# Performance work log

Measured on AMD Instinct MI355X. Metric: run time of the kernel, lower is better.

Reference implementation:

```python
import jax, jax.numpy as jnp
import numpy as np

HUMAN_IDX = 0
SCORE_TH = 0.2
NMS_TH = 0.5
MIN_H, MAX_H = 3, 15
MIN_O, MAX_O = 3, 15
NEG = -1e9


def cxcywh_to_xyxy(b):
    cx, cy, w, h = jnp.split(b, 4, axis=-1)
    return jnp.concatenate([cx - 0.5 * w, cy - 0.5 * h, cx + 0.5 * w, cy + 0.5 * h], -1)


def pairwise_iou(a, b):
    # torchvision-style IoU treating last-dim-4 as xyxy (areas unclamped, mimics
    # batched_nms being fed cxcywh boxes exactly as the original module does).
    lt = jnp.maximum(a[:, None, :2], b[None, :, :2])
    rb = jnp.minimum(a[:, None, 2:], b[None, :, 2:])
    wh = jnp.clip(rb - lt, 0.0)
    inter = wh[..., 0] * wh[..., 1]
    area_a = (a[:, 2] - a[:, 0]) * (a[:, 3] - a[:, 1])
    area_b = (b[:, 2] - b[:, 0]) * (b[:, 3] - b[:, 1])
    union = area_a[:, None] + area_b[None, :] - inter
    return inter / jnp.where(union == 0, 1.0, union)


def nms_keep(boxes, scores, labels, iou_th):
    # batched_nms via the class-offset trick, greedy suppression in score order
    Q = boxes.shape[0]
    off = labels.astype(boxes.dtype)[:, None] * (boxes.max() + 1.0)
    b = boxes + off
    order = jnp.argsort(-scores)
    bs = b[order]
    iou = pairwise_iou(bs, bs)                      # [Q,Q]
    later = jnp.arange(Q)[None, :] > jnp.arange(Q)[:, None]
    sup_mat = (iou > iou_th) & later

    def body(i, keep):
        return keep & ~(sup_mat[i] & keep[i])

    keep_sorted = jax.lax.fori_loop(0, Q, body, jnp.ones(Q, dtype=bool))
    return jnp.zeros(Q, dtype=bool).at[order].set(keep_sorted)


def decode_boxes(b, d):
    # BoxPairCoder-style delta decode on normalized cxcywh boxes
    cx, cy, w, h = b[:, 0], b[:, 1], b[:, 2], b[:, 3]
    cx2 = cx + d[:, 0] * w
    cy2 = cy + d[:, 1] * h
    w2 = w * jnp.exp(d[:, 2])
    h2 = h * jnp.exp(d[:, 3])
    return jnp.stack([cx2, cy2, w2, h2], -1)


def per_image(logits, boxes, hs, size, Wv, bv, Wb, bb):
    prob = jax.nn.softmax(logits, -1)
    scores = prob[:, :-1].max(-1)
    labels = jnp.argmax(prob[:, :-1], -1)
    keep = nms_keep(boxes, scores, labels, NMS_TH)

    is_h = labels == HUMAN_IDX
    h_sc = jnp.where(keep & is_h, scores, NEG)
    o_sc = jnp.where(keep & ~is_h, scores, NEG)
    n_h = jnp.sum(keep & is_h & (scores >= SCORE_TH))
    n_o = jnp.sum(keep & ~is_h & (scores >= SCORE_TH))
    k_h = jnp.clip(n_h, MIN_H, MAX_H)
    k_o = jnp.clip(n_o, MIN_O, MAX_O)

    top_h_sc, idx_h = jax.lax.top_k(h_sc, MAX_H)
    top_o_sc, idx_o = jax.lax.top_k(o_sc, MAX_O)
    val_h = (jnp.arange(MAX_H) < k_h) & (top_h_sc > NEG / 2)
    val_o = (jnp.arange(MAX_O) < k_o) & (top_o_sc > NEG / 2)

    # all human-object pairs [P = MAX_H*MAX_O]
    ih = jnp.repeat(idx_h, MAX_O)
    io = jnp.tile(idx_o, MAX_H)
    pair_valid = jnp.repeat(val_h, MAX_O) & jnp.tile(val_o, MAX_H)

    feat = jnp.concatenate([hs[ih], hs[io]], -1)    # [P, 2D]
    vlog = feat @ Wv + bv                           # verb logits [P, V]
    delta = feat @ Wb + bb                          # box-pair deltas [P, 8]

    pr = (jnp.repeat(jnp.where(val_h, top_h_sc, 0.0), MAX_O)
          * jnp.tile(jnp.where(val_o, top_o_sc, 0.0), MAX_H))
    pr = jnp.where(pair_valid, pr, 0.0)

    bh = decode_boxes(boxes[ih], delta[:, :4])
    bo = decode_boxes(boxes[io], delta[:, 4:])

    hgt, wid = size[0], size[1]
    scale = jnp.stack([wid, hgt, wid, hgt])
    kept = jnp.concatenate([idx_h, idx_o])
    boxes_out = cxcywh_to_xyxy(boxes[kept]) * scale
    bh_out = cxcywh_to_xyxy(bh) * scale
    bo_out = cxcywh_to_xyxy(bo) * scale
    det_scores = jax.nn.sigmoid(vlog) * pr[:, None]
    return boxes_out, bh_out, bo_out, det_scores


def setup_inputs() -> dict:
    key = jax.random.key(0)
    ks = jax.random.split(key, 6)
    B, Q, C1, D, V = 64, 900, 81, 256, 117
    return {
        "pred_logits": jax.random.normal(ks[0], (B, Q, C1), jnp.float32),
        "pred_boxes": jax.random.uniform(ks[1], (B, Q, 4), jnp.float32),
        "hidden_states": jax.random.normal(ks[2], (B, Q, D), jnp.float32),
        "image_sizes": jax.random.uniform(ks[3], (B, 2), jnp.float32) * 1000.0 + 300.0,
        "W_verb": jax.random.normal(ks[4], (2 * D, V), jnp.float32) * 0.02,
        "b_verb": jnp.zeros((V,), jnp.float32),
        "W_bbox": jax.random.normal(ks[5], (2 * D, 8), jnp.float32) * 0.02,
        "b_bbox": jnp.zeros((8,), jnp.float32),
    }


def reference(pred_logits, pred_boxes, hidden_states, image_sizes, W_verb, b_verb, W_bbox, b_bbox):
    f = jax.vmap(per_image, in_axes=(0, 0, 0, 0, None, None, None, None))
    return f(pred_logits, pred_boxes, hidden_states, image_sizes, W_verb, b_verb, W_bbox, b_bbox)
```

## Files before the change

kernel.cpp:

```cpp
#include <hip/hip_runtime.h>
#include <math.h>

#define NB 64
#define Q 900
#define NC 81
#define NC2 80
#define HD 256
#define NV 117
#define NEGV -1000000000.0f

static const size_t OFF_SCORES = 0;
static const size_t OFF_LABELS = 230400;
static const size_t OFF_HSC    = 460800;
static const size_t OFF_OSC    = 691200;

typedef float float4u __attribute__((ext_vector_type(4), aligned(4)));

__global__ __launch_bounds__(256) void k_score(const float* __restrict__ logits,
                                               float* __restrict__ scores,
                                               int* __restrict__ labels) {
  int quad = threadIdx.x >> 2, qq = threadIdx.x & 3;
  int row = blockIdx.x * 64 + quad;
  const float* lp = logits + (size_t)row * NC;
  float4u x[5];
  #pragma unroll
  for (int j = 0; j < 5; j++) {
    int c = qq + 4 * j;
    x[j] = *(const float4u*)(lp + c * 4);
  }
  float x80 = (qq == 0) ? lp[80] : -INFINITY;
  float m = x80;
  #pragma unroll
  for (int j = 0; j < 5; j++)
    m = fmaxf(m, fmaxf(fmaxf(x[j].x, x[j].y), fmaxf(x[j].z, x[j].w)));
  m = fmaxf(m, __shfl_xor(m, 1));
  m = fmaxf(m, __shfl_xor(m, 2));
  float e = (qq == 0) ? expf(x80 - m) : 0.0f;
  #pragma unroll
  for (int j = 0; j < 5; j++)
    e += expf(x[j].x - m) + expf(x[j].y - m) + expf(x[j].z - m) + expf(x[j].w - m);
  e += __shfl_xor(e, 1);
  e += __shfl_xor(e, 2);
  float bv = -INFINITY; int bi = 0x7fffffff;
  #pragma unroll
  for (int j = 0; j < 5; j++) {
    int base = (qq + 4 * j) * 4;
    if (x[j].x > bv) { bv = x[j].x; bi = base; }
    if (x[j].y > bv) { bv = x[j].y; bi = base + 1; }
    if (x[j].z > bv) { bv = x[j].z; bi = base + 2; }
    if (x[j].w > bv) { bv = x[j].w; bi = base + 3; }
  }
  #pragma unroll
  for (int s = 1; s <= 2; s <<= 1) {
    float ov = __shfl_xor(bv, s); int oi = __shfl_xor(bi, s);
    if (ov > bv || (ov == bv && oi < bi)) { bv = ov; bi = oi; }
  }
  if (qq == 0) {
    scores[row] = expf(bv - m) / e;
    labels[row] = bi;
  }
}

__global__ __launch_bounds__(512) void k_cnms(const float* __restrict__ scores,
                                              const int* __restrict__ labels,
                                              const float* __restrict__ boxes,
                                              float* __restrict__ hsc,
                                              float* __restrict__ osc) {
#pragma clang fp contract(off)
  int img = blockIdx.x;
  int tid = threadIdx.x;
  int wid = tid >> 6, lane = tid & 63;
  int c = blockIdx.y * 8 + wid;
  size_t imgQ = (size_t)img * Q;
  __shared__ float  s_sc[8][64];
  __shared__ int    s_idx[8][64];
  __shared__ int    s_srt[8][64];
  __shared__ float  s_ssc[8][64];
  __shared__ float4 s_sb[8][64];
  __shared__ unsigned long long s_sup[8][64];
  __shared__ float  s_wmax[8];

  const float4* bp4 = (const float4*)(boxes + imgQ * 4);
  float bm = -INFINITY;
  for (int i = tid; i < Q; i += 512) {
    float4 v = bp4[i];
    bm = fmaxf(bm, fmaxf(fmaxf(v.x, v.y), fmaxf(v.z, v.w)));
  }
  #pragma unroll
  for (int s = 32; s > 0; s >>= 1) bm = fmaxf(bm, __shfl_xor(bm, s));
  if (lane == 0) s_wmax[wid] = bm;
  __syncthreads();
  float bmax = s_wmax[0];
  #pragma unroll
  for (int i = 1; i < 8; i++) bmax = fmaxf(bmax, s_wmax[i]);

  int lb[15]; float sc[15];
  #pragma unroll
  for (int e = 0; e < 15; e++) {
    int i = e * 64 + lane;
    lb[e] = (i < Q) ? labels[imgQ + i] : -1;
    sc[e] = (i < Q) ? scores[imgQ + i] : 0.0f;
  }
  unsigned long long lmask = (1ull << lane) - 1ull;
  int n = 0;
  #pragma unroll
  for (int e = 0; e < 15; e++) {
    bool memb = (lb[e] == c);
    unsigned long long mm = __ballot(memb);
    if (memb) {
      int pos = n + __popcll(mm & lmask);
      if (pos < 64) { s_idx[wid][pos] = e * 64 + lane; s_sc[wid][pos] = sc[e]; }
    }
    n += __popcll(mm);
  }
  n = min(n, 64);

  int   myidx = (lane < n) ? s_idx[wid][lane] : 0;
  float mysc  = (lane < n) ? s_sc[wid][lane]  : -INFINITY;

  int rank = 0;
  #pragma unroll 4
  for (int j = 0; j < n; j++) {
    float sj = s_sc[wid][j];
    rank += (sj > mysc) || (sj == mysc && j < lane);
  }

  if (lane < n) {
    float off = (float)c * (bmax + 1.0f);
    const float* bp = boxes + (imgQ + myidx) * 4;
    float4 b;
    b.x = bp[0] + off; b.y = bp[1] + off;
    b.z = bp[2] + off; b.w = bp[3] + off;
    s_srt[wid][rank] = myidx;
    s_ssc[wid][rank] = mysc;
    s_sb[wid][rank]  = b;
  }

  float4 mb = (lane < n) ? s_sb[wid][lane] : float4{0.f, 0.f, 0.f, 0.f};
  float areaA = (mb.z - mb.x) * (mb.w - mb.y);

  unsigned long long sup = 0;
  #pragma unroll 4
  for (int j = 0; j < n; j++) {
    float4 cb = s_sb[wid][j];
    if (j > lane && lane < n) {
      float ltx = fmaxf(mb.x, cb.x), lty = fmaxf(mb.y, cb.y);
      float rbx = fminf(mb.z, cb.z), rby = fminf(mb.w, cb.w);
      float ww = fmaxf(rbx - ltx, 0.0f), hh = fmaxf(rby - lty, 0.0f);
      float inter = ww * hh;
      float areaB = (cb.z - cb.x) * (cb.w - cb.y);
      float uni = areaA + areaB - inter;
      float denom = (uni == 0.0f) ? 1.0f : uni;
      if (inter / denom > 0.5f) sup |= (1ull << j);
    }
  }
  s_sup[wid][lane] = sup;

  unsigned long long keepm = (n >= 64) ? ~0ull : ((1ull << n) - 1ull);
  #pragma unroll 4
  for (int i = 0; i < n; i++) {
    unsigned long long row = s_sup[wid][i];
    if ((keepm >> i) & 1ull) keepm &= ~row;
  }

  if (lane < n) {
    int kept = (int)((keepm >> lane) & 1ull);
    int   oi = s_srt[wid][lane];
    float os = s_ssc[wid][lane];
    hsc[imgQ + oi] = (kept && c == 0) ? os : NEGV;
    osc[imgQ + oi] = (kept && c != 0) ? os : NEGV;
  }
}

__global__ __launch_bounds__(512) void k_back(const float* __restrict__ hscg,
                                              const float* __restrict__ oscg,
                                              const float* __restrict__ boxes,
                                              const float* __restrict__ hs,
                                              const float* __restrict__ sizes,
                                              const float* __restrict__ Wv,
                                              const float* __restrict__ bverb,
                                              const float* __restrict__ Wb,
                                              const float* __restrict__ bbox,
                                              float* __restrict__ out) {
  int slice = blockIdx.x, img = blockIdx.y;
  int t = threadIdx.x, w = t >> 6, lane = t & 63;
  size_t imgQ = (size_t)img * Q;

  __shared__ __attribute__((aligned(16))) float s_A[30 * 260];
  __shared__ float s_B[2][64][16];
  __shared__ float s_Cg[30][16];
  __shared__ int   s_tki[30];
  __shared__ float s_tkv[30];
  __shared__ int   s_tkval[30];
  __shared__ float s_pr[225];
  __shared__ float s_box30[120];

  if (w < 2) {
    const float* src = (w == 0) ? hscg : oscg;
    float v[15];
    int cnt = 0;
    #pragma unroll
    for (int e = 0; e < 15; e++) {
      int i = e * 64 + lane;
      float val = (i < Q) ? src[imgQ + i] : -INFINITY;
      cnt += (val >= 0.2f) ? 1 : 0;
      v[e] = val;
    }
    #pragma unroll
    for (int s = 32; s > 0; s >>= 1) cnt += __shfl_xor(cnt, s);

    float selv = 0.f; int seli = 0;
    for (int r = 0; r < 15; r++) {
      float bv_ = -INFINITY; int bi_ = 0x7fffffff;
      #pragma unroll
      for (int e = 0; e < 15; e++) { if (v[e] > bv_) { bv_ = v[e]; bi_ = e * 64 + lane; } }
      #pragma unroll
      for (int s = 32; s > 0; s >>= 1) {
        float ov = __shfl_xor(bv_, s); int oi2 = __shfl_xor(bi_, s);
        if (ov > bv_ || (ov == bv_ && oi2 < bi_)) { bv_ = ov; bi_ = oi2; }
      }
      if (lane == r) { selv = bv_; seli = bi_; }
      if ((bi_ & 63) == lane) {
        int ee = bi_ >> 6;
        #pragma unroll
        for (int e = 0; e < 15; e++) if (e == ee) v[e] = -2.0e9f;
      }
    }
    int kk = min(max(cnt, 3), 15);
    if (lane < 15) {
      s_tki[w * 15 + lane]   = seli;
      s_tkv[w * 15 + lane]   = selv;
      s_tkval[w * 15 + lane] = (lane < kk && selv > -5.0e8f) ? 1 : 0;
    }
  }
  __syncthreads();

  if (t < 225) {
    int h_ = t / 15, o_ = t - h_ * 15;
    float th = s_tkv[h_], to_ = s_tkv[15 + o_];
    s_pr[t] = (s_tkval[h_] && s_tkval[15 + o_]) ? th * to_ : 0.0f;
  }
  if (t < 120) {
    int r = t >> 2, j = t & 3;
    s_box30[t] = boxes[(imgQ + s_tki[r]) * 4 + j];
  }

  for (int f = t; f < 1920; f += 512) {
    int r = f >> 6, q = f & 63;
    float4 a = *(const float4*)(hs + (imgQ + s_tki[r]) * HD + q * 4);
    ((float4*)s_A)[r * 65 + q] = a;
  }

  int r = t >> 4, c = t & 15;
  float acc = 0.0f;
  for (int kc = 0; kc < 256; kc += 64) {
    __syncthreads();
    for (int idx = t; idx < 2048; idx += 512) {
      int half = idx >> 10, rem = idx & 1023;
      int k_l = rem >> 4, c_l = rem & 15;
      int pcol = slice * 16 + c_l;
      int kg = kc + k_l + (half ? 256 : 0);
      float val = 0.0f;
      if (pcol < 117)      val = Wv[(size_t)kg * 117 + pcol];
      else if (pcol < 125) val = Wb[(size_t)kg * 8 + (pcol - 117)];
      s_B[half][k_l][c_l] = val;
    }
    __syncthreads();
    if (r < 30) {
      const float* Bp = &s_B[r < 15 ? 0 : 1][0][0];
      #pragma unroll
      for (int kk = 0; kk < 64; kk += 4) {
        float4 a4 = *(const float4*)(s_A + r * 260 + kc + kk);
        acc += a4.x * Bp[(kk + 0) * 16 + c];
        acc += a4.y * Bp[(kk + 1) * 16 + c];
        acc += a4.z * Bp[(kk + 2) * 16 + c];
        acc += a4.w * Bp[(kk + 3) * 16 + c];
      }
    }
  }
  if (r < 30) s_Cg[r][c] = acc;
  __syncthreads();

  float hgt = sizes[img * 2 + 0], wid = sizes[img * 2 + 1];
  float* out0 = out;
  float* out1 = out + 7680;
  float* out2 = out + 65280;
  float* out3 = out + 122880;

  int veff = (slice < 7) ? 16 : 5;
  for (int e = t; e < 225 * veff; e += 512) {
    int p = e / veff, cl = e - p * veff;
    int ph = p / 15, po = p - ph * 15;
    int v = slice * 16 + cl;
    float x = s_Cg[ph][cl] + s_Cg[15 + po][cl] + bverb[v];
    out3[(size_t)img * 26325 + p * NV + v] = (1.0f / (1.0f + expf(-x))) * s_pr[p];
  }

  if (slice == 7) {
    if (t < 30) {
      const float* bp = s_box30 + t * 4;
      float cx = bp[0], cy = bp[1], ww = bp[2], hh = bp[3];
      float* o = out0 + ((size_t)img * 30 + t) * 4;
      o[0] = (cx - 0.5f * ww) * wid;
      o[1] = (cy - 0.5f * hh) * hgt;
      o[2] = (cx + 0.5f * ww) * wid;
      o[3] = (cy + 0.5f * hh) * hgt;
    }
    if (t < 225) {
      int h_ = t / 15, o_ = t - h_ * 15;
      {
        float d0 = s_Cg[h_][5] + s_Cg[15 + o_][5] + bbox[0];
        float d1 = s_Cg[h_][6] + s_Cg[15 + o_][6] + bbox[1];
        float d2 = s_Cg[h_][7] + s_Cg[15 + o_][7] + bbox[2];
        float d3 = s_Cg[h_][8] + s_Cg[15 + o_][8] + bbox[3];
        const float* bp = s_box30 + h_ * 4;
        float cx = bp[0], cy = bp[1], ww = bp[2], hh = bp[3];
        float cx2 = cx + d0 * ww, cy2 = cy + d1 * hh;
        float w2 = ww * expf(d2), h2 = hh * expf(d3);
        float* o = out1 + ((size_t)img * 225 + t) * 4;
        o[0] = (cx2 - 0.5f * w2) * wid;
        o[1] = (cy2 - 0.5f * h2) * hgt;
        o[2] = (cx2 + 0.5f * w2) * wid;
        o[3] = (cy2 + 0.5f * h2) * hgt;
      }
      {
        float d4 = s_Cg[h_][9]  + s_Cg[15 + o_][9]  + bbox[4];
        float d5 = s_Cg[h_][10] + s_Cg[15 + o_][10] + bbox[5];
        float d6 = s_Cg[h_][11] + s_Cg[15 + o_][11] + bbox[6];
        float d7 = s_Cg[h_][12] + s_Cg[15 + o_][12] + bbox[7];
        const float* bp = s_box30 + (15 + o_) * 4;
        float cx = bp[0], cy = bp[1], ww = bp[2], hh = bp[3];
        float cx2 = cx + d4 * ww, cy2 = cy + d5 * hh;
        float w2 = ww * expf(d6), h2 = hh * expf(d7);
        float* o = out2 + ((size_t)img * 225 + t) * 4;
        o[0] = (cx2 - 0.5f * w2) * wid;
        o[1] = (cy2 - 0.5f * h2) * hgt;
        o[2] = (cx2 + 0.5f * w2) * wid;
        o[3] = (cy2 + 0.5f * h2) * hgt;
      }
    }
  }
}

extern "C" void kernel_launch(void* const* d_in, const int* in_sizes, int n_in,
                              void* d_out, int out_size, void* d_ws, size_t ws_size,
                              hipStream_t stream) {
  const float* logits = (const float*)d_in[0];
  const float* boxes  = (const float*)d_in[1];
  const float* hs     = (const float*)d_in[2];
  const float* sizes  = (const float*)d_in[3];
  const float* Wv     = (const float*)d_in[4];
  const float* bv     = (const float*)d_in[5];
  const float* Wb     = (const float*)d_in[6];
  const float* bb     = (const float*)d_in[7];
  float* out = (float*)d_out;
  char* ws = (char*)d_ws;

  float* scores = (float*)(ws + OFF_SCORES);
  int*   labels = (int*)(ws + OFF_LABELS);
  float* hsc    = (float*)(ws + OFF_HSC);
  float* osc    = (float*)(ws + OFF_OSC);

  k_score<<<900, 256, 0, stream>>>(logits, scores, labels);
  k_cnms<<<dim3(NB, 10), 512, 0, stream>>>(scores, labels, boxes, hsc, osc);
  k_back<<<dim3(8, NB), 512, 0, stream>>>(hsc, osc, boxes, hs, sizes,
                                          Wv, bv, Wb, bb, out);
}
```

Baseline: 54.20 us.

## Fuse score, class-NMS and backend into one persistent kernel with grid barriers

Merges the three kernels into a single 512-block persistent kernel that runs scoring, per-class NMS and the pair head as phases separated by software grid barriers built on atomics, with a memset to reset the barrier counters. The per-image box max moves to a global buffer, and the GEMM is reworked for 256-thread blocks, each thread accumulating two rows. The aim is to remove the inter-kernel launch gaps and tail effects. In exchange it adds barrier spin cost and depends on all 512 blocks being co-resident (launch bounds request 3 blocks per CU); if they are not, the barrier only exits through its guard counter.

```diff
diff --git a/kernel.cpp b/kernel.cpp
--- a/kernel.cpp
+++ b/kernel.cpp
@@ -8,335 +8,378 @@
 #define HD 256
 #define NV 117
 #define NEGV -1000000000.0f
+#define GRID 512
+#define BLK 256
 
 static const size_t OFF_SCORES = 0;
 static const size_t OFF_LABELS = 230400;
 static const size_t OFF_HSC    = 460800;
 static const size_t OFF_OSC    = 691200;
+static const size_t OFF_BMAX   = 921600;
+static const size_t OFF_BAR    = 922112;
 
 typedef float float4u __attribute__((ext_vector_type(4), aligned(4)));
 
-__global__ __launch_bounds__(256) void k_score(const float* __restrict__ logits,
-                                               float* __restrict__ scores,
-                                               int* __restrict__ labels) {
-  int quad = threadIdx.x >> 2, qq = threadIdx.x & 3;
-  int row = blockIdx.x * 64 + quad;
-  const float* lp = logits + (size_t)row * NC;
-  float4u x[5];
-  #pragma unroll
-  for (int j = 0; j < 5; j++) {
-    int c = qq + 4 * j;
-    x[j] = *(const float4u*)(lp + c * 4);
+__device__ __forceinline__ void gridbar(int* cnt, int* flag) {
+  __syncthreads();
+  if (threadIdx.x == 0) {
+    __threadfence();
+    int prev = atomicAdd(cnt, 1);
+    if (prev == GRID - 1) {
+      __hip_atomic_store(flag, 1, __ATOMIC_RELEASE, __HIP_MEMORY_SCOPE_AGENT);
+    } else {
+      int guard = 0;
+      while (__hip_atomic_load(flag, __ATOMIC_ACQUIRE, __HIP_MEMORY_SCOPE_AGENT) == 0
+             && guard < (1 << 24)) {
+        guard++;
+        __builtin_amdgcn_s_sleep(2);
+      }
+    }
+    __threadfence();
   }
-  float x80 = (qq == 0) ? lp[80] : -INFINITY;
-  float m = x80;
-  #pragma unroll
-  for (int j = 0; j < 5; j++)
-    m = fmaxf(m, fmaxf(fmaxf(x[j].x, x[j].y), fmaxf(x[j].z, x[j].w)));
-  m = fmaxf(m, __shfl_xor(m, 1));
-  m = fmaxf(m, __shfl_xor(m, 2));
-  float e = (qq == 0) ? expf(x80 - m) : 0.0f;
-  #pragma unroll
-  for (int j = 0; j < 5; j++)
-    e += expf(x[j].x - m) + expf(x[j].y - m) + expf(x[j].z - m) + expf(x[j].w - m);
-  e += __shfl_xor(e, 1);
-  e += __shfl_xor(e, 2);
-  float bv = -INFINITY; int bi = 0x7fffffff;
-  #pragma unroll
-  for (int j = 0; j < 5; j++) {
-    int base = (qq + 4 * j) * 4;
-    if (x[j].x > bv) { bv = x[j].x; bi = base; }
-    if (x[j].y > bv) { bv = x[j].y; bi = base + 1; }
-    if (x[j].z > bv) { bv = x[j].z; bi = base + 2; }
-    if (x[j].w > bv) { bv = x[j].w; bi = base + 3; }
-  }
-  #pragma unroll
-  for (int s = 1; s <= 2; s <<= 1) {
-    float ov = __shfl_xor(bv, s); int oi = __shfl_xor(bi, s);
-    if (ov > bv || (ov == bv && oi < bi)) { bv = ov; bi = oi; }
-  }
-  if (qq == 0) {
-    scores[row] = expf(bv - m) / e;
-    labels[row] = bi;
-  }
+  __syncthreads();
 }
 
-__global__ __launch_bounds__(512) void k_cnms(const float* __restrict__ scores,
-                                              const int* __restrict__ labels,
-                                              const float* __restrict__ boxes,
-                                              float* __restrict__ hsc,
-                                              float* __restrict__ osc) {
-#pragma clang fp contract(off)
-  int img = blockIdx.x;
-  int tid = threadIdx.x;
-  int wid = tid >> 6, lane = tid & 63;
-  int c = blockIdx.y * 8 + wid;
-  size_t imgQ = (size_t)img * Q;
-  __shared__ float  s_sc[8][64];
-  __shared__ int    s_idx[8][64];
-  __shared__ int    s_srt[8][64];
-  __shared__ float  s_ssc[8][64];
-  __shared__ float4 s_sb[8][64];
-  __shared__ unsigned long long s_sup[8][64];
-  __shared__ float  s_wmax[8];
-
-  const float4* bp4 = (const float4*)(boxes + imgQ * 4);
-  float bm = -INFINITY;
-  for (int i = tid; i < Q; i += 512) {
-    float4 v = bp4[i];
-    bm = fmaxf(bm, fmaxf(fmaxf(v.x, v.y), fmaxf(v.z, v.w)));
-  }
-  #pragma unroll
-  for (int s = 32; s > 0; s >>= 1) bm = fmaxf(bm, __shfl_xor(bm, s));
-  if (lane == 0) s_wmax[wid] = bm;
-  __syncthreads();
-  float bmax = s_wmax[0];
-  #pragma unroll
-  for (int i = 1; i < 8; i++) bmax = fmaxf(bmax, s_wmax[i]);
-
-  int lb[15]; float sc[15];
-  #pragma unroll
-  for (int e = 0; e < 15; e++) {
-    int i = e * 64 + lane;
-    lb[e] = (i < Q) ? labels[imgQ + i] : -1;
-    sc[e] = (i < Q) ? scores[imgQ + i] : 0.0f;
-  }
-  unsigned long long lmask = (1ull << lane) - 1ull;
-  int n = 0;
-  #pragma unroll
-  for (int e = 0; e < 15; e++) {
-    bool memb = (lb[e] == c);
-    unsigned long long mm = __ballot(memb);
-    if (memb) {
-      int pos = n + __popcll(mm & lmask);
-      if (pos < 64) { s_idx[wid][pos] = e * 64 + lane; s_sc[wid][pos] = sc[e]; }
-    }
-    n += __popcll(mm);
-  }
-  n = min(n, 64);
-
-  int   myidx = (lane < n) ? s_idx[wid][lane] : 0;
-  float mysc  = (lane < n) ? s_sc[wid][lane]  : -INFINITY;
-
-  int rank = 0;
-  #pragma unroll 4
-  for (int j = 0; j < n; j++) {
-    float sj = s_sc[wid][j];
-    rank += (sj > mysc) || (sj == mysc && j < lane);
-  }
-
-  if (lane < n) {
-    float off = (float)c * (bmax + 1.0f);
-    const float* bp = boxes + (imgQ + myidx) * 4;
-    float4 b;
-    b.x = bp[0] + off; b.y = bp[1] + off;
-    b.z = bp[2] + off; b.w = bp[3] + off;
-    s_srt[wid][rank] = myidx;
-    s_ssc[wid][rank] = mysc;
-    s_sb[wid][rank]  = b;
-  }
-
-  float4 mb = (lane < n) ? s_sb[wid][lane] : float4{0.f, 0.f, 0.f, 0.f};
-  float areaA = (mb.z - mb.x) * (mb.w - mb.y);
-
-  unsigned long long sup = 0;
-  #pragma unroll 4
-  for (int j = 0; j < n; j++) {
-    float4 cb = s_sb[wid][j];
-    if (j > lane && lane < n) {
-      float ltx = fmaxf(mb.x, cb.x), lty = fmaxf(mb.y, cb.y);
-      float rbx = fminf(mb.z, cb.z), rby = fminf(mb.w, cb.w);
-      float ww = fmaxf(rbx - ltx, 0.0f), hh = fmaxf(rby - lty, 0.0f);
-      float inter = ww * hh;
-      float areaB = (cb.z - cb.x) * (cb.w - cb.y);
-      float uni = areaA + areaB - inter;
-      float denom = (uni == 0.0f) ? 1.0f : uni;
-      if (inter / denom > 0.5f) sup |= (1ull << j);
-    }
-  }
-  s_sup[wid][lane] = sup;
-
-  unsigned long long keepm = (n >= 64) ? ~0ull : ((1ull << n) - 1ull);
-  #pragma unroll 4
-  for (int i = 0; i < n; i++) {
-    unsigned long long row = s_sup[wid][i];
-    if ((keepm >> i) & 1ull) keepm &= ~row;
-  }
-
-  if (lane < n) {
-    int kept = (int)((keepm >> lane) & 1ull);
-    int   oi = s_srt[wid][lane];
-    float os = s_ssc[wid][lane];
-    hsc[imgQ + oi] = (kept && c == 0) ? os : NEGV;
-    osc[imgQ + oi] = (kept && c != 0) ? os : NEGV;
-  }
-}
-
-__global__ __launch_bounds__(512) void k_back(const float* __restrict__ hscg,
-                                              const float* __restrict__ oscg,
-                                              const float* __restrict__ boxes,
-                                              const float* __restrict__ hs,
-                                              const float* __restrict__ sizes,
-                                              const float* __restrict__ Wv,
-                                              const float* __restrict__ bverb,
-                                              const float* __restrict__ Wb,
-                                              const float* __restrict__ bbox,
-                                              float* __restrict__ out) {
-  int slice = blockIdx.x, img = blockIdx.y;
-  int t = threadIdx.x, w = t >> 6, lane = t & 63;
-  size_t imgQ = (size_t)img * Q;
-
-  __shared__ __attribute__((aligned(16))) float s_A[30 * 260];
-  __shared__ float s_B[2][64][16];
-  __shared__ float s_Cg[30][16];
+__global__ __launch_bounds__(BLK, 3) void k_all(const float* __restrict__ logits,
+                                                const float* __restrict__ boxes,
+                                                const float* __restrict__ hs,
+                                                const float* __restrict__ sizes,
+                                                const float* __restrict__ Wv,
+                                                const float* __restrict__ bverb,
+                                                const float* __restrict__ Wb,
+                                                const float* __restrict__ bbox,
+                                                float* __restrict__ scores,
+                                                int* __restrict__ labels,
+                                                float* __restrict__ hsc,
+                                                float* __restrict__ osc,
+                                                float* __restrict__ bmaxg,
+                                                int* __restrict__ bar,
+                                                float* __restrict__ out) {
+  int b = blockIdx.x, t = threadIdx.x;
+  int w = t >> 6, lane = t & 63;
+
+  __shared__ __attribute__((aligned(16))) float u_mem[10328];
+  __shared__ float s_red[4];
   __shared__ int   s_tki[30];
   __shared__ float s_tkv[30];
   __shared__ int   s_tkval[30];
   __shared__ float s_pr[225];
   __shared__ float s_box30[120];
 
-  if (w < 2) {
-    const float* src = (w == 0) ? hscg : oscg;
-    float v[15];
-    int cnt = 0;
-    #pragma unroll
-    for (int e = 0; e < 15; e++) {
-      int i = e * 64 + lane;
-      float val = (i < Q) ? src[imgQ + i] : -INFINITY;
-      cnt += (val >= 0.2f) ? 1 : 0;
-      v[e] = val;
-    }
-    #pragma unroll
-    for (int s = 32; s > 0; s >>= 1) cnt += __shfl_xor(cnt, s);
-
-    float selv = 0.f; int seli = 0;
-    for (int r = 0; r < 15; r++) {
-      float bv_ = -INFINITY; int bi_ = 0x7fffffff;
-      #pragma unroll
-      for (int e = 0; e < 15; e++) { if (v[e] > bv_) { bv_ = v[e]; bi_ = e * 64 + lane; } }
-      #pragma unroll
-      for (int s = 32; s > 0; s >>= 1) {
-        float ov = __shfl_xor(bv_, s); int oi2 = __shfl_xor(bi_, s);
-        if (ov > bv_ || (ov == bv_ && oi2 < bi_)) { bv_ = ov; bi_ = oi2; }
-      }
-      if (lane == r) { selv = bv_; seli = bi_; }
-      if ((bi_ & 63) == lane) {
-        int ee = bi_ >> 6;
+  {
+    for (int gt = b * BLK + t; gt < NB * Q * 4; gt += GRID * BLK) {
+      int gq = gt >> 2, qq = gt & 3;
+      const float* lp = logits + (size_t)gq * NC;
+      float4u x[5];
+      #pragma unroll
+      for (int j = 0; j < 5; j++) {
+        int c = qq + 4 * j;
+        x[j] = *(const float4u*)(lp + c * 4);
+      }
+      float x80 = (qq == 0) ? lp[80] : -INFINITY;
+      float m = x80;
+      #pragma unroll
+      for (int j = 0; j < 5; j++)
+        m = fmaxf(m, fmaxf(fmaxf(x[j].x, x[j].y), fmaxf(x[j].z, x[j].w)));
+      m = fmaxf(m, __shfl_xor(m, 1));
+      m = fmaxf(m, __shfl_xor(m, 2));
+      float e = (qq == 0) ? expf(x80 - m) : 0.0f;
+      #pragma unroll
+      for (int j = 0; j < 5; j++)
+        e += expf(x[j].x - m) + expf(x[j].y - m) + expf(x[j].z - m) + expf(x[j].w - m);
+      e += __shfl_xor(e, 1);
+      e += __shfl_xor(e, 2);
+      float bv = -INFINITY; int bi = 0x7fffffff;
+      #pragma unroll
+      for (int j = 0; j < 5; j++) {
+        int base = (qq + 4 * j) * 4;
+        if (x[j].x > bv) { bv = x[j].x; bi = base; }
+        if (x[j].y > bv) { bv = x[j].y; bi = base + 1; }
+        if (x[j].z > bv) { bv = x[j].z; bi = base + 2; }
+        if (x[j].w > bv) { bv = x[j].w; bi = base + 3; }
+      }
+      #pragma unroll
+      for (int s = 1; s <= 2; s <<= 1) {
+        float ov = __shfl_xor(bv, s); int oi = __shfl_xor(bi, s);
+        if (ov > bv || (ov == bv && oi < bi)) { bv = ov; bi = oi; }
+      }
+      if (qq == 0) {
+        scores[gq] = expf(bv - m) / e;
+        labels[gq] = bi;
+      }
+    }
+    if (b >= GRID - NB) {
+      int img = b - (GRID - NB);
+      const float4* bp4 = (const float4*)(boxes + (size_t)img * Q * 4);
+      float bm = -INFINITY;
+      for (int i = t; i < Q; i += BLK) {
+        float4 v = bp4[i];
+        bm = fmaxf(bm, fmaxf(fmaxf(v.x, v.y), fmaxf(v.z, v.w)));
+      }
+      #pragma unroll
+      for (int s = 32; s > 0; s >>= 1) bm = fmaxf(bm, __shfl_xor(bm, s));
+      if (lane == 0) s_red[w] = bm;
+      __syncthreads();
+      if (t == 0) {
+        float mm = fmaxf(fmaxf(s_red[0], s_red[1]), fmaxf(s_red[2], s_red[3]));
+        bmaxg[img] = mm;
+      }
+    }
+  }
+  gridbar(bar + 0, bar + 32);
+
+  {
+#pragma clang fp contract(off)
+    float* wbase = u_mem + w * 512;
+    int*    w_idx = (int*)wbase;
+    float*  w_sc  = wbase + 64;
+    float4* w_box = (float4*)(wbase + 128);
+    unsigned long long* w_sup = (unsigned long long*)(wbase + 384);
+    unsigned long long lmask = (1ull << lane) - 1ull;
+
+    for (int pp = b * 10 + w; pp < b * 10 + 10; pp += 4) {
+      int img = pp / 80, c = pp - img * 80;
+      size_t imgQ = (size_t)img * Q;
+      float bmax = bmaxg[img];
+
+      int lb[15]; float sc[15];
+      #pragma unroll
+      for (int e = 0; e < 15; e++) {
+        int i = e * 64 + lane;
+        lb[e] = (i < Q) ? labels[imgQ + i] : -1;
+        sc[e] = (i < Q) ? scores[imgQ + i] : 0.0f;
+      }
+      int n = 0;
+      #pragma unroll
+      for (int e = 0; e < 15; e++) {
+        bool memb = (lb[e] == c);
+        unsigned long long mm = __ballot(memb);
+        if (memb) {
+          int pos = n + __popcll(mm & lmask);
+          if (pos < 64) { w_idx[pos] = e * 64 + lane; w_sc[pos] = sc[e]; }
+        }
+        n += __popcll(mm);
+      }
+      n = min(n, 64);
+
+      int   myidx = (lane < n) ? w_idx[lane] : 0;
+      float mysc  = (lane < n) ? w_sc[lane]  : -INFINITY;
+
+      int rank = 0;
+      #pragma unroll 4
+      for (int j = 0; j < n; j++) {
+        float sj = w_sc[j];
+        rank += (sj > mysc) || (sj == mysc && j < lane);
+      }
+
+      if (lane < n) {
+        float off = (float)c * (bmax + 1.0f);
+        const float* bp = boxes + (imgQ + myidx) * 4;
+        float4 bx;
+        bx.x = bp[0] + off; bx.y = bp[1] + off;
+        bx.z = bp[2] + off; bx.w = bp[3] + off;
+        w_idx[rank] = myidx;
+        w_sc[rank]  = mysc;
+        w_box[rank] = bx;
+      }
+
+      float4 mb = (lane < n) ? w_box[lane] : float4{0.f, 0.f, 0.f, 0.f};
+      float areaA = (mb.z - mb.x) * (mb.w - mb.y);
+
+      unsigned long long sup = 0;
+      #pragma unroll 4
+      for (int j = 0; j < n; j++) {
+        float4 cb = w_box[j];
+        if (j > lane && lane < n) {
+          float ltx = fmaxf(mb.x, cb.x), lty = fmaxf(mb.y, cb.y);
+          float rbx = fminf(mb.z, cb.z), rby = fminf(mb.w, cb.w);
+          float ww = fmaxf(rbx - ltx, 0.0f), hh = fmaxf(rby - lty, 0.0f);
+          float inter = ww * hh;
+          float areaB = (cb.z - cb.x) * (cb.w - cb.y);
+          float uni = areaA + areaB - inter;
+          float denom = (uni == 0.0f) ? 1.0f : uni;
+          if (inter / denom > 0.5f) sup |= (1ull << j);
+        }
+      }
+      w_sup[lane] = sup;
+
+      unsigned long long keepm = (n >= 64) ? ~0ull : ((1ull << n) - 1ull);
+      #pragma unroll 4
+      for (int i = 0; i < n; i++) {
+        unsigned long long row = w_sup[i];
+        if ((keepm >> i) & 1ull) keepm &= ~row;
+      }
+
+      if (lane < n) {
+        int kept = (int)((keepm >> lane) & 1ull);
+        int   oi = w_idx[lane];
+        float os = w_sc[lane];
+        hsc[imgQ + oi] = (kept && c == 0) ? os : NEGV;
+        osc[imgQ + oi] = (kept && c != 0) ? os : NEGV;
+      }
+    }
+  }
+  gridbar(bar + 64, bar + 96);
+
+  {
+    int slice = b & 7, img = b >> 3;
+    size_t imgQ = (size_t)img * Q;
+    float* s_A  = u_mem;
+    float* s_B  = u_mem + 7800;
+    float* s_Cg = u_mem + 9848;
+
+    if (w < 2) {
+      const float* src = (w == 0) ? hsc : osc;
+      float v[15];
+      int cnt = 0;
+      #pragma unroll
+      for (int e = 0; e < 15; e++) {
+        int i = e * 64 + lane;
+        float val = (i < Q) ? src[imgQ + i] : -INFINITY;
+        cnt += (val >= 0.2f) ? 1 : 0;
+        v[e] = val;
+      }
+      #pragma unroll
+      for (int s = 32; s > 0; s >>= 1) cnt += __shfl_xor(cnt, s);
+
+      float selv = 0.f; int seli = 0;
+      for (int r = 0; r < 15; r++) {
+        float bv_ = -INFINITY; int bi_ = 0x7fffffff;
         #pragma unroll
-        for (int e = 0; e < 15; e++) if (e == ee) v[e] = -2.0e9f;
-      }
-    }
-    int kk = min(max(cnt, 3), 15);
-    if (lane < 15) {
-      s_tki[w * 15 + lane]   = seli;
-      s_tkv[w * 15 + lane]   = selv;
-      s_tkval[w * 15 + lane] = (lane < kk && selv > -5.0e8f) ? 1 : 0;
-    }
-  }
-  __syncthreads();
-
-  if (t < 225) {
-    int h_ = t / 15, o_ = t - h_ * 15;
-    float th = s_tkv[h_], to_ = s_tkv[15 + o_];
-    s_pr[t] = (s_tkval[h_] && s_tkval[15 + o_]) ? th * to_ : 0.0f;
-  }
-  if (t < 120) {
-    int r = t >> 2, j = t & 3;
-    s_box30[t] = boxes[(imgQ + s_tki[r]) * 4 + j];
-  }
-
-  for (int f = t; f < 1920; f += 512) {
-    int r = f >> 6, q = f & 63;
-    float4 a = *(const float4*)(hs + (imgQ + s_tki[r]) * HD + q * 4);
-    ((float4*)s_A)[r * 65 + q] = a;
-  }
-
-  int r = t >> 4, c = t & 15;
-  float acc = 0.0f;
-  for (int kc = 0; kc < 256; kc += 64) {
+        for (int e = 0; e < 15; e++) { if (v[e] > bv_) { bv_ = v[e]; bi_ = e * 64 + lane; } }
+        #pragma unroll
+        for (int s = 32; s > 0; s >>= 1) {
+          float ov = __shfl_xor(bv_, s); int oi2 = __shfl_xor(bi_, s);
+          if (ov > bv_ || (ov == bv_ && oi2 < bi_)) { bv_ = ov; bi_ = oi2; }
+        }
+        if (lane == r) { selv = bv_; seli = bi_; }
+        if ((bi_ & 63) == lane) {
+          int ee = bi_ >> 6;
+          #pragma unroll
+          for (int e = 0; e < 15; e++) if (e == ee) v[e] = -2.0e9f;
+        }
+      }
+      int kk = min(max(cnt, 3), 15);
+      if (lane < 15) {
+        s_tki[w * 15 + lane]   = seli;
+        s_tkv[w * 15 + lane]   = selv;
+        s_tkval[w * 15 + lane] = (lane < kk && selv > -5.0e8f) ? 1 : 0;
+      }
+    }
     __syncthreads();
-    for (int idx = t; idx < 2048; idx += 512) {
-      int half = idx >> 10, rem = idx & 1023;
-      int k_l = rem >> 4, c_l = rem & 15;
-      int pcol = slice * 16 + c_l;
-      int kg = kc + k_l + (half ? 256 : 0);
-      float val = 0.0f;
-      if (pcol < 117)      val = Wv[(size_t)kg * 117 + pcol];
-      else if (pcol < 125) val = Wb[(size_t)kg * 8 + (pcol - 117)];
-      s_B[half][k_l][c_l] = val;
-    }
-    __syncthreads();
-    if (r < 30) {
-      const float* Bp = &s_B[r < 15 ? 0 : 1][0][0];
-      #pragma unroll
-      for (int kk = 0; kk < 64; kk += 4) {
-        float4 a4 = *(const float4*)(s_A + r * 260 + kc + kk);
-        acc += a4.x * Bp[(kk + 0) * 16 + c];
-        acc += a4.y * Bp[(kk + 1) * 16 + c];
-        acc += a4.z * Bp[(kk + 2) * 16 + c];
-        acc += a4.w * Bp[(kk + 3) * 16 + c];
-      }
-    }
-  }
-  if (r < 30) s_Cg[r][c] = acc;
-  __syncthreads();
-
-  float hgt = sizes[img * 2 + 0], wid = sizes[img * 2 + 1];
-  float* out0 = out;
-  float* out1 = out + 7680;
-  float* out2 = out + 65280;
-  float* out3 = out + 122880;
-
-  int veff = (slice < 7) ? 16 : 5;
-  for (int e = t; e < 225 * veff; e += 512) {
-    int p = e / veff, cl = e - p * veff;
-    int ph = p / 15, po = p - ph * 15;
-    int v = slice * 16 + cl;
-    float x = s_Cg[ph][cl] + s_Cg[15 + po][cl] + bverb[v];
-    out3[(size_t)img * 26325 + p * NV + v] = (1.0f / (1.0f + expf(-x))) * s_pr[p];
-  }
-
-  if (slice == 7) {
-    if (t < 30) {
-      const float* bp = s_box30 + t * 4;
-      float cx = bp[0], cy = bp[1], ww = bp[2], hh = bp[3];
-      float* o = out0 + ((size_t)img * 30 + t) * 4;
-      o[0] = (cx - 0.5f * ww) * wid;
-      o[1] = (cy - 0.5f * hh) * hgt;
-      o[2] = (cx + 0.5f * ww) * wid;
-      o[3] = (cy + 0.5f * hh) * hgt;
-    }
+
     if (t < 225) {
       int h_ = t / 15, o_ = t - h_ * 15;
-      {
-        float d0 = s_Cg[h_][5] + s_Cg[15 + o_][5] + bbox[0];
-        float d1 = s_Cg[h_][6] + s_Cg[15 + o_][6] + bbox[1];
-        float d2 = s_Cg[h_][7] + s_Cg[15 + o_][7] + bbox[2];
-        float d3 = s_Cg[h_][8] + s_Cg[15 + o_][8] + bbox[3];
-        const float* bp = s_box30 + h_ * 4;
+      float th = s_tkv[h_], to_ = s_tkv[15 + o_];
+      s_pr[t] = (s_tkval[h_] && s_tkval[15 + o_]) ? th * to_ : 0.0f;
+    }
+    if (t < 120) {
+      int r = t >> 2, j = t & 3;
+      s_box30[t] = boxes[(imgQ + s_tki[r]) * 4 + j];
+    }
+
+    for (int f = t; f < 1920; f += BLK) {
+      int r = f >> 6, q = f & 63;
+      float4 a = *(const float4*)(hs + (imgQ + s_tki[r]) * HD + q * 4);
+      ((float4*)s_A)[r * 65 + q] = a;
+    }
+
+    int r0 = t >> 4, c = t & 15;
+    int r1 = r0 + 16;
+    bool has1 = (r1 < 30);
+    float acc0 = 0.0f, acc1 = 0.0f;
+    for (int kc = 0; kc < 256; kc += 64) {
+      __syncthreads();
+      for (int idx = t; idx < 2048; idx += BLK) {
+        int half = idx >> 10, rem = idx & 1023;
+        int k_l = rem >> 4, c_l = rem & 15;
+        int pcol = slice * 16 + c_l;
+        int kg = kc + k_l + (half ? 256 : 0);
+        float val = 0.0f;
+        if (pcol < 117)      val = Wv[(size_t)kg * 117 + pcol];
+        else if (pcol < 125) val = Wb[(size_t)kg * 8 + (pcol - 117)];
+        s_B[half * 1024 + k_l * 16 + c_l] = val;
+      }
+      __syncthreads();
+      const float* Bp0 = s_B + (r0 < 15 ? 0 : 1024);
+      const float* Bp1 = s_B + 1024;
+      #pragma unroll
+      for (int kk = 0; kk < 64; kk += 4) {
+        float4 a0 = *(const float4*)(s_A + r0 * 260 + kc + kk);
+        acc0 += a0.x * Bp0[(kk + 0) * 16 + c];
+        acc0 += a0.y * Bp0[(kk + 1) * 16 + c];
+        acc0 += a0.z * Bp0[(kk + 2) * 16 + c];
+        acc0 += a0.w * Bp0[(kk + 3) * 16 + c];
+        if (has1) {
+          float4 a1 = *(const float4*)(s_A + r1 * 260 + kc + kk);
+          acc1 += a1.x * Bp1[(kk + 0) * 16 + c];
+          acc1 += a1.y * Bp1[(kk + 1) * 16 + c];
+          acc1 += a1.z * Bp1[(kk + 2) * 16 + c];
+          acc1 += a1.w * Bp1[(kk + 3) * 16 + c];
+        }
+      }
+    }
+    s_Cg[r0 * 16 + c] = acc0;
+    if (has1) s_Cg[r1 * 16 + c] = acc1;
+    __syncthreads();
+
+    float hgt = sizes[img * 2 + 0], wid = sizes[img * 2 + 1];
+    float* out0 = out;
+    float* out1 = out + 7680;
+    float* out2 = out + 65280;
+    float* out3 = out + 122880;
+
+    int veff = (slice < 7) ? 16 : 5;
+    for (int e = t; e < 225 * veff; e += BLK) {
+      int p = e / veff, cl = e - p * veff;
+      int ph = p / 15, po = p - ph * 15;
+      int v = slice * 16 + cl;
+      float x = s_Cg[ph * 16 + cl] + s_Cg[(15 + po) * 16 + cl] + bverb[v];
+      out3[(size_t)img * 26325 + p * NV + v] = (1.0f / (1.0f + expf(-x))) * s_pr[p];
+    }
+
+    if (slice == 7) {
+      if (t < 30) {
+        const float* bp = s_box30 + t * 4;
         float cx = bp[0], cy = bp[1], ww = bp[2], hh = bp[3];
-        float cx2 = cx + d0 * ww, cy2 = cy + d1 * hh;
-        float w2 = ww * expf(d2), h2 = hh * expf(d3);
-        float* o = out1 + ((size_t)img * 225 + t) * 4;
-        o[0] = (cx2 - 0.5f * w2) * wid;
-        o[1] = (cy2 - 0.5f * h2) * hgt;
-        o[2] = (cx2 + 0.5f * w2) * wid;
-        o[3] = (cy2 + 0.5f * h2) * hgt;
-      }
-      {
-        float d4 = s_Cg[h_][9]  + s_Cg[15 + o_][9]  + bbox[4];
-        float d5 = s_Cg[h_][10] + s_Cg[15 + o_][10] + bbox[5];
-        float d6 = s_Cg[h_][11] + s_Cg[15 + o_][11] + bbox[6];
-        float d7 = s_Cg[h_][12] + s_Cg[15 + o_][12] + bbox[7];
-        const float* bp = s_box30 + (15 + o_) * 4;
-        float cx = bp[0], cy = bp[1], ww = bp[2], hh = bp[3];
-        float cx2 = cx + d4 * ww, cy2 = cy + d5 * hh;
-        float w2 = ww * expf(d6), h2 = hh * expf(d7);
-        float* o = out2 + ((size_t)img * 225 + t) * 4;
-        o[0] = (cx2 - 0.5f * w2) * wid;
-        o[1] = (cy2 - 0.5f * h2) * hgt;
-        o[2] = (cx2 + 0.5f * w2) * wid;
-        o[3] = (cy2 + 0.5f * h2) * hgt;
+        float* o = out0 + ((size_t)img * 30 + t) * 4;
+        o[0] = (cx - 0.5f * ww) * wid;
+        o[1] = (cy - 0.5f * hh) * hgt;
+        o[2] = (cx + 0.5f * ww) * wid;
+        o[3] = (cy + 0.5f * hh) * hgt;
+      }
+      if (t < 225) {
+        int h_ = t / 15, o_ = t - h_ * 15;
+        {
+          float d0 = s_Cg[h_ * 16 + 5] + s_Cg[(15 + o_) * 16 + 5] + bbox[0];
+          float d1 = s_Cg[h_ * 16 + 6] + s_Cg[(15 + o_) * 16 + 6] + bbox[1];
+          float d2 = s_Cg[h_ * 16 + 7] + s_Cg[(15 + o_) * 16 + 7] + bbox[2];
+          float d3 = s_Cg[h_ * 16 + 8] + s_Cg[(15 + o_) * 16 + 8] + bbox[3];
+          const float* bp = s_box30 + h_ * 4;
+          float cx = bp[0], cy = bp[1], ww = bp[2], hh = bp[3];
+          float cx2 = cx + d0 * ww, cy2 = cy + d1 * hh;
+          float w2 = ww * expf(d2), h2 = hh * expf(d3);
+          float* o = out1 + ((size_t)img * 225 + t) * 4;
+          o[0] = (cx2 - 0.5f * w2) * wid;
+          o[1] = (cy2 - 0.5f * h2) * hgt;
+          o[2] = (cx2 + 0.5f * w2) * wid;
+          o[3] = (cy2 + 0.5f * h2) * hgt;
+        }
+        {
+          float d4 = s_Cg[h_ * 16 + 9]  + s_Cg[(15 + o_) * 16 + 9]  + bbox[4];
+          float d5 = s_Cg[h_ * 16 + 10] + s_Cg[(15 + o_) * 16 + 10] + bbox[5];
+          float d6 = s_Cg[h_ * 16 + 11] + s_Cg[(15 + o_) * 16 + 11] + bbox[6];
+          float d7 = s_Cg[h_ * 16 + 12] + s_Cg[(15 + o_) * 16 + 12] + bbox[7];
+          const float* bp = s_box30 + (15 + o_) * 4;
+          float cx = bp[0], cy = bp[1], ww = bp[2], hh = bp[3];
+          float cx2 = cx + d4 * ww, cy2 = cy + d5 * hh;
+          float w2 = ww * expf(d6), h2 = hh * expf(d7);
+          float* o = out2 + ((size_t)img * 225 + t) * 4;
+          o[0] = (cx2 - 0.5f * w2) * wid;
+          o[1] = (cy2 - 0.5f * h2) * hgt;
+          o[2] = (cx2 + 0.5f * w2) * wid;
+          o[3] = (cy2 + 0.5f * h2) * hgt;
+        }
       }
     }
   }
@@ -360,9 +403,10 @@
   int*   labels = (int*)(ws + OFF_LABELS);
   float* hsc    = (float*)(ws + OFF_HSC);
   float* osc    = (float*)(ws + OFF_OSC);
-
-  k_score<<<900, 256, 0, stream>>>(logits, scores, labels);
-  k_cnms<<<dim3(NB, 10), 512, 0, stream>>>(scores, labels, boxes, hsc, osc);
-  k_back<<<dim3(8, NB), 512, 0, stream>>>(hsc, osc, boxes, hs, sizes,
-                                          Wv, bv, Wb, bb, out);
+  float* bmaxg  = (float*)(ws + OFF_BMAX);
+  int*   bar    = (int*)(ws + OFF_BAR);
+
+  hipMemsetAsync(ws + OFF_BAR, 0, 512, stream);
+  k_all<<<GRID, BLK, 0, stream>>>(logits, boxes, hs, sizes, Wv, bv, Wb, bb,
+                                  scores, labels, hsc, osc, bmaxg, bar, out);
 }
```

Result: slower. 137.6 us (+154.0%).
